# Kernel tuning notes

Hardware: AMD Instinct MI355X
Metric: run time of the kernel (lower is better)

## Reference

```python
import jax, jax.numpy as jnp
import numpy as np

N = 50000      # nodes
E = 300000     # edges
B = 256        # graphs
F = 128        # feat_dim
F2 = 256       # gnn width = 2*feat_dim
Q = 64         # qubit_num
A = 2016       # action_num
L = 10         # SAGEConv layers
NEG = 0.01     # leaky_relu slope
EPS = 1e-5


def _leaky(v):
    return jnp.where(v > 0, v, NEG * v)


def setup_inputs() -> dict:
    key = jax.random.key(0)
    ks = jax.random.split(key, 16)
    s = 0.05
    x = jax.random.randint(ks[0], (N, 2), 0, Q + 1)
    edge_index = jax.random.randint(ks[1], (2, E), 0, N)
    batch = jnp.sort(jax.random.randint(ks[2], (N,), 0, B))
    emb = (jax.random.normal(ks[3], (Q + 1, F)) * s).at[0].set(0.0)  # padding_idx=0
    Wl = jax.random.normal(ks[4], (L, F2, F2)) * s   # SAGEConv lin_l (neighbor)
    bl = jnp.zeros((L, F2))
    Wr = jax.random.normal(ks[5], (L, F2, F2)) * s   # SAGEConv lin_r (root), no bias
    gn_weight = jnp.ones((F2,))
    gn_bias = jnp.zeros((F2,))
    gn_scale = jnp.ones((F2,))                        # GraphNorm mean_scale
    t = jnp.array(1.0, dtype=jnp.float32)             # SoftmaxAggregation temperature
    W1 = jax.random.normal(ks[6], (F2, F2)) * s
    b1 = jnp.zeros((F2,))
    W2 = jax.random.normal(ks[7], (F2, F)) * s
    b2 = jnp.zeros((F,))
    W3 = jax.random.normal(ks[8], (F, A)) * s
    b3 = jnp.zeros((A,))
    return dict(x=x, edge_index=edge_index, batch=batch, emb=emb, Wl=Wl, bl=bl,
                Wr=Wr, gn_weight=gn_weight, gn_bias=gn_bias, gn_scale=gn_scale,
                t=t, W1=W1, b1=b1, W2=W2, b2=b2, W3=W3, b3=b3)


def reference(x, edge_index, batch, emb, Wl, bl, Wr, gn_weight, gn_bias,
              gn_scale, t, W1, b1, W2, b2, W3, b3):
    # node embedding: two qubit tokens per node -> [N, 2F] = [N, F2]
    h = emb.at[0].set(0.0)[x].reshape(-1, F2)
    src, dst = edge_index[0], edge_index[1]
    deg = jax.ops.segment_sum(jnp.ones((E,), h.dtype), dst, num_segments=N)
    deg = jnp.maximum(deg, 1.0)[:, None]
    for i in range(L):
        agg = jax.ops.segment_sum(h[src], dst, num_segments=N) / deg  # [N, F2]
        h2 = agg @ Wl[i] + bl[i] + h @ Wr[i]
        h = _leaky(h2) + h2
    # GraphNorm (per-graph mean/var with learnable mean_scale)
    cnt = jnp.maximum(jax.ops.segment_sum(jnp.ones((N,), h.dtype), batch,
                                          num_segments=B), 1.0)[:, None]
    mean = jax.ops.segment_sum(h, batch, num_segments=B) / cnt
    o = h - mean[batch] * gn_scale
    var = jax.ops.segment_sum(o * o, batch, num_segments=B) / cnt
    h = gn_weight * o / jnp.sqrt(var + EPS)[batch] + gn_bias
    # SoftmaxAggregation (per-graph, per-channel segment softmax weights)
    logits = h * t
    m = jax.ops.segment_max(logits, batch, num_segments=B)
    ex = jnp.exp(logits - m[batch])
    den = jax.ops.segment_sum(ex, batch, num_segments=B)
    alpha = ex / den[batch]
    g = jax.ops.segment_sum(alpha * h, batch, num_segments=B)  # [B, F2]
    # MLP head
    y = _leaky(g @ W1 + b1)
    y = _leaky(y @ W2 + b2)
    return y @ W3 + b3  # [B, A]
```

## Files before the change

kernel.cpp:

```cpp
#include <hip/hip_runtime.h>

typedef unsigned short u16;
typedef __bf16 bf16x8 __attribute__((ext_vector_type(8)));
typedef float floatx4 __attribute__((ext_vector_type(4)));

#define NN 50000
#define EE 300000
#define BB 256
#define MPAD 50048
#define CAP 32
#define AA 2016
#define EB ((EE + 255) / 256)

__device__ __forceinline__ float b2f(u16 u) {
    union { float f; unsigned int i; } x; x.i = ((unsigned int)u) << 16; return x.f;
}
__device__ __forceinline__ float lo16(unsigned int w) {
    union { float f; unsigned int i; } x; x.i = w << 16; return x.f;
}
__device__ __forceinline__ float hi16(unsigned int w) {
    union { float f; unsigned int i; } x; x.i = w & 0xffff0000u; return x.f;
}
__device__ __forceinline__ u16 f2b(float f) {
    union { float f; unsigned int i; } x; x.f = f;
    unsigned int r = (x.i + 0x7fffu + ((x.i >> 16) & 1u)) >> 16;
    return (u16)r;
}
__device__ __forceinline__ int sniff(const u16* tp) {
    return (tp[0] == 0x3F80u) ? 0 : 1;
}
__device__ __forceinline__ float loadf(const void* p, size_t i, int md) {
    return md ? ((const float*)p)[i] : b2f(((const u16*)p)[i]);
}

typedef const void __attribute__((address_space(1)))* gas_ptr;
typedef void __attribute__((address_space(3)))* las_ptr;
#define ASYNC_COPY16(gp, lp) \
    __builtin_amdgcn_global_load_lds((gas_ptr)(const void*)(gp), (las_ptr)(void*)(lp), 16, 0, 0)

__global__ __launch_bounds__(256) void embed_kernel(const int* __restrict__ x,
                                                    const void* __restrict__ emb,
                                                    const u16* __restrict__ tp,
                                                    u16* __restrict__ h,
                                                    int* __restrict__ cur) {
    int md = sniff(tp);
    int idx = blockIdx.x * 256 + threadIdx.x;
    if (idx < NN) cur[idx] = 0;
    int n = idx >> 6, lane = idx & 63;
    int c4 = lane * 4;
    int which = (c4 >> 7) & 1;
    int tok = x[n * 2 + which];
    int ec = c4 & 127;
    size_t ei = (size_t)tok * 128 + ec;
    float e0, e1, e2, e3;
    if (md) {
        float4 v = *(const float4*)((const float*)emb + ei);
        e0 = v.x; e1 = v.y; e2 = v.z; e3 = v.w;
    } else {
        ushort4 v = *(const ushort4*)((const u16*)emb + ei);
        e0 = b2f(v.x); e1 = b2f(v.y); e2 = b2f(v.z); e3 = b2f(v.w);
    }
    ushort4 o;
    o.x = f2b(e0); o.y = f2b(e1); o.z = f2b(e2); o.w = f2b(e3);
    *(ushort4*)&h[(size_t)n * 256 + c4] = o;
}

__global__ __launch_bounds__(256) void scatter_kernel(const int* __restrict__ src,
                                                      const int* __restrict__ dst,
                                                      const int* __restrict__ batch,
                                                      int* __restrict__ cur,
                                                      int* __restrict__ csrc,
                                                      int* __restrict__ goff) {
    int i = blockIdx.x * 256 + threadIdx.x;
    if (i < EE) {
        int d = dst[i];
        int slot = atomicAdd(&cur[d], 1);
        if (slot < CAP) csrc[(size_t)d * CAP + slot] = src[i];
    }
    if (blockIdx.x == EB) {
        for (int t = threadIdx.x; t <= BB; t += 256) {
            int lo = 0, hi = NN;
            while (lo < hi) {
                int mid = (lo + hi) >> 1;
                if (batch[mid] < t) lo = mid + 1; else hi = mid;
            }
            goff[t] = lo;
        }
    }
}

__global__ __launch_bounds__(256) void transpose_kernel(const void* __restrict__ Wl,
                                                        const void* __restrict__ Wr,
                                                        const u16* __restrict__ tp,
                                                        u16* __restrict__ Wt) {
    __shared__ float tile[32][33];
    int md = sniff(tp);
    int w2 = blockIdx.z;
    const void* Ws = (w2 & 1) ? Wr : Wl;
    size_t base = (size_t)(w2 >> 1) * 65536;
    u16* Wo = Wt + (size_t)w2 * 65536;
    int kt = blockIdx.y * 32, nt = blockIdx.x * 32;
    int tx = threadIdx.x, ty = threadIdx.y;
#pragma unroll
    for (int q = 0; q < 4; ++q)
        tile[ty + q * 8][tx] = loadf(Ws, base + (size_t)(kt + ty + q * 8) * 256 + nt + tx, md);
    __syncthreads();
#pragma unroll
    for (int q = 0; q < 4; ++q)
        Wo[(size_t)(nt + ty + q * 8) * 256 + kt + tx] = f2b(tile[tx][ty + q * 8]);
}

__global__ __launch_bounds__(256) void agg_kernel(const u16* __restrict__ h,
                                                  const int* __restrict__ cur,
                                                  const int* __restrict__ csrc,
                                                  u16* __restrict__ agg) {
    int node = blockIdx.x * 4 + (threadIdx.x >> 6);
    int lane = threadIdx.x & 63;
    int half = lane >> 5, l32 = lane & 31;
    int cd = cur[node];
    float id = 1.0f / (float)(cd > 1 ? cd : 1);
    int cnt = cd > CAP ? CAP : cd;
    const int s = node * CAP;
    const int e = s + cnt;
    float a[8] = {};
    int p = s + half;
    for (; p + 2 < e; p += 4) {
        int sn0 = csrc[p];
        int sn1 = csrc[p + 2];
        uint4 h0 = *(const uint4*)&h[(size_t)sn0 * 256 + l32 * 8];
        uint4 h1 = *(const uint4*)&h[(size_t)sn1 * 256 + l32 * 8];
        a[0] += lo16(h0.x) + lo16(h1.x); a[1] += hi16(h0.x) + hi16(h1.x);
        a[2] += lo16(h0.y) + lo16(h1.y); a[3] += hi16(h0.y) + hi16(h1.y);
        a[4] += lo16(h0.z) + lo16(h1.z); a[5] += hi16(h0.z) + hi16(h1.z);
        a[6] += lo16(h0.w) + lo16(h1.w); a[7] += hi16(h0.w) + hi16(h1.w);
    }
    if (p < e) {
        int sn = csrc[p];
        uint4 hv = *(const uint4*)&h[(size_t)sn * 256 + l32 * 8];
        a[0] += lo16(hv.x); a[1] += hi16(hv.x);
        a[2] += lo16(hv.y); a[3] += hi16(hv.y);
        a[4] += lo16(hv.z); a[5] += hi16(hv.z);
        a[6] += lo16(hv.w); a[7] += hi16(hv.w);
    }
#pragma unroll
    for (int j = 0; j < 8; ++j) a[j] += __shfl_xor(a[j], 32, 64);
    if (half == 0) {
        u16 o[8];
#pragma unroll
        for (int j = 0; j < 8; ++j) o[j] = f2b(a[j] * id);
        *(uint4*)&agg[(size_t)node * 256 + l32 * 8] = *(uint4*)o;
    }
}

__global__ __launch_bounds__(512, 4) void gemm_kernel(const u16* __restrict__ A0,
                                                      const u16* __restrict__ A1,
                                                      const u16* __restrict__ B0,
                                                      const u16* __restrict__ B1,
                                                      const void* __restrict__ blv,
                                                      int layer,
                                                      const u16* __restrict__ tp,
                                                      u16* __restrict__ Hout) {
    __shared__ __align__(16) u16 As[2][128 * 32];
    __shared__ __align__(16) u16 Bs[2][256 * 32];
    int md = sniff(tp);
    const int tid = threadIdx.x;
    const int lane = tid & 63;
    const int wv = tid >> 6;
    const int wm = wv >> 2, wn = wv & 3;
    const int m0 = blockIdx.x * 128;
    const int r16 = lane & 15, q = lane >> 4;
    const int rg = lane >> 2;
    const int slot = lane & 3;

    floatx4 acc[4][4] = {};

    auto issue = [&](int kt, int p) {
        const u16* __restrict__ Asrc = (kt < 8) ? A0 : A1;
        const u16* __restrict__ Bsrc = (kt < 8) ? B0 : B1;
        const int koff = (kt & 7) * 32;
        {
            int row = wv * 16 + rg;
            int g = slot ^ ((row >> 1) & 3);
            int ga = m0 + row; if (ga > NN - 1) ga = NN - 1;
            ASYNC_COPY16(Asrc + (size_t)ga * 256 + koff + g * 8,
                         &As[p][(wv * 16) * 32]);
        }
#pragma unroll
        for (int i = 0; i < 2; ++i) {
            int row = wv * 32 + i * 16 + rg;
            int g = slot ^ ((row >> 1) & 3);
            ASYNC_COPY16(Bsrc + (size_t)row * 256 + koff + g * 8,
                         &Bs[p][(wv * 32 + i * 16) * 32]);
        }
    };

    issue(0, 0);
    for (int kt = 0; kt < 16; ++kt) {
        __syncthreads();
        if (kt < 15) issue(kt + 1, (kt + 1) & 1);
        const int p = kt & 1;
        bf16x8 av[4], bv[4];
#pragma unroll
        for (int mt = 0; mt < 4; ++mt) {
            int row = wm * 64 + mt * 16 + r16;
            int pc = q ^ ((row >> 1) & 3);
            av[mt] = *(const bf16x8*)&As[p][row * 32 + pc * 8];
        }
#pragma unroll
        for (int nt = 0; nt < 4; ++nt) {
            int row = wn * 64 + nt * 16 + r16;
            int pc = q ^ ((row >> 1) & 3);
            bv[nt] = *(const bf16x8*)&Bs[p][row * 32 + pc * 8];
        }
#pragma unroll
        for (int mt = 0; mt < 4; ++mt)
#pragma unroll
            for (int nt = 0; nt < 4; ++nt)
                acc[mt][nt] = __builtin_amdgcn_mfma_f32_16x16x32_bf16(
                    bv[nt], av[mt], acc[mt][nt], 0, 0, 0);
    }
#pragma unroll
    for (int nt = 0; nt < 4; ++nt) {
        int gn = wn * 64 + nt * 16 + q * 4;
        float b0 = loadf(blv, (size_t)layer * 256 + gn + 0, md);
        float b1 = loadf(blv, (size_t)layer * 256 + gn + 1, md);
        float b2 = loadf(blv, (size_t)layer * 256 + gn + 2, md);
        float b3 = loadf(blv, (size_t)layer * 256 + gn + 3, md);
#pragma unroll
        for (int mt = 0; mt < 4; ++mt) {
            int gm = m0 + wm * 64 + mt * 16 + r16;
            if (gm < NN) {
                float v0 = acc[mt][nt][0] + b0;
                float v1 = acc[mt][nt][1] + b1;
                float v2 = acc[mt][nt][2] + b2;
                float v3 = acc[mt][nt][3] + b3;
                v0 = (v0 > 0.f) ? 2.f * v0 : 1.01f * v0;
                v1 = (v1 > 0.f) ? 2.f * v1 : 1.01f * v1;
                v2 = (v2 > 0.f) ? 2.f * v2 : 1.01f * v2;
                v3 = (v3 > 0.f) ? 2.f * v3 : 1.01f * v3;
                ushort4 o;
                o.x = f2b(v0); o.y = f2b(v1); o.z = f2b(v2); o.w = f2b(v3);
                *(ushort4*)&Hout[(size_t)gm * 256 + gn] = o;
            }
        }
    }
}

__global__ __launch_bounds__(1024) void gn_softmax_kernel(const u16* __restrict__ h,
                                                          const int* __restrict__ goff,
                                                          const void* __restrict__ gnw,
                                                          const void* __restrict__ gnb,
                                                          const void* __restrict__ gns,
                                                          const u16* __restrict__ tp,
                                                          float* __restrict__ g) {
    __shared__ float red[1024];
    __shared__ float red2[1024];
    int md = sniff(tp);
    const int sub = threadIdx.x >> 8;
    const int c = threadIdx.x & 255;
    const int b = blockIdx.x;
    const int s = goff[b], e = goff[b + 1];
    const int cn = e - s;
    const float icnt = 1.0f / (float)(cn > 1 ? cn : 1);

    float sum = 0.f, sq = 0.f;
#pragma unroll 4
    for (int n = s + sub; n < e; n += 4) {
        float hv = b2f(h[(size_t)n * 256 + c]);
        sum += hv; sq += hv * hv;
    }
    red[threadIdx.x] = sum; red2[threadIdx.x] = sq; __syncthreads();
    float mean = (red[c] + red[256 + c] + red[512 + c] + red[768 + c]) * icnt;
    float e2 = (red2[c] + red2[256 + c] + red2[512 + c] + red2[768 + c]) * icnt;
    float msc = mean * loadf(gns, c, md);
    float var = e2 - 2.f * msc * mean + msc * msc;
    if (var < 0.f) var = 0.f;
    float w = loadf(gnw, c, md) * rsqrtf(var + 1e-5f);
    float bb = loadf(gnb, c, md);
    float tv = md ? ((const float*)tp)[0] : b2f(tp[0]);
    __syncthreads();

    float den = 0.f, num = 0.f;
#pragma unroll 4
    for (int n = s + sub; n < e; n += 4) {
        float hn = w * (b2f(h[(size_t)n * 256 + c]) - msc) + bb;
        float elv = __expf(fminf(hn * tv, 60.f));
        den += elv; num += elv * hn;
    }
    red[threadIdx.x] = den; red2[threadIdx.x] = num; __syncthreads();
    if (sub == 0) {
        float D = red[c] + red[256 + c] + red[512 + c] + red[768 + c];
        float Nu = red2[c] + red2[256 + c] + red2[512 + c] + red2[768 + c];
        g[b * 256 + c] = (D > 1e-30f) ? (Nu / D) : 0.f;
    }
}

__global__ __launch_bounds__(256) void y1_kernel(const float* __restrict__ g,
                                                 const void* __restrict__ W1,
                                                 const void* __restrict__ b1,
                                                 const u16* __restrict__ tp,
                                                 float* __restrict__ y1) {
    __shared__ float gr[256];
    int md = sniff(tp);
    int row = blockIdx.x, t = threadIdx.x;
    gr[t] = g[row * 256 + t];
    __syncthreads();
    float acc = 0.f;
    if (md) {
        const float* W = (const float*)W1;
#pragma unroll 8
        for (int k = 0; k < 256; ++k) acc += gr[k] * W[(size_t)k * 256 + t];
    } else {
        const u16* W = (const u16*)W1;
#pragma unroll 8
        for (int k = 0; k < 256; ++k) acc += gr[k] * b2f(W[(size_t)k * 256 + t]);
    }
    float v = acc + loadf(b1, t, md);
    y1[row * 256 + t] = (v > 0.f) ? v : 0.01f * v;
}

__global__ __launch_bounds__(128) void y2_kernel(const float* __restrict__ y1,
                                                 const void* __restrict__ W2,
                                                 const void* __restrict__ b2v,
                                                 const u16* __restrict__ tp,
                                                 float* __restrict__ y2) {
    __shared__ float yr[256];
    int md = sniff(tp);
    int row = blockIdx.x, t = threadIdx.x;
    yr[t] = y1[row * 256 + t];
    yr[t + 128] = y1[row * 256 + t + 128];
    __syncthreads();
    float acc = 0.f;
    if (md) {
        const float* W = (const float*)W2;
#pragma unroll 8
        for (int k = 0; k < 256; ++k) acc += yr[k] * W[(size_t)k * 128 + t];
    } else {
        const u16* W = (const u16*)W2;
#pragma unroll 8
        for (int k = 0; k < 256; ++k) acc += yr[k] * b2f(W[(size_t)k * 128 + t]);
    }
    float v = acc + loadf(b2v, t, md);
    y2[row * 128 + t] = (v > 0.f) ? v : 0.01f * v;
}

__global__ __launch_bounds__(256) void out_kernel(const float* __restrict__ y2,
                                                  const void* __restrict__ W3,
                                                  const void* __restrict__ b3,
                                                  const u16* __restrict__ tp,
                                                  void* __restrict__ outp) {
    __shared__ float yr[128];
    int md = sniff(tp);
    int row = blockIdx.y;
    int col = blockIdx.x * 256 + threadIdx.x;
    if (threadIdx.x < 128) yr[threadIdx.x] = y2[row * 128 + threadIdx.x];
    __syncthreads();
    if (col >= AA) return;
    float acc = 0.f;
    if (md) {
        const float* W = (const float*)W3;
#pragma unroll 8
        for (int k = 0; k < 128; ++k) acc += yr[k] * W[(size_t)k * AA + col];
    } else {
        const u16* W = (const u16*)W3;
#pragma unroll 8
        for (int k = 0; k < 128; ++k) acc += yr[k] * b2f(W[(size_t)k * AA + col]);
    }
    float v = acc + loadf(b3, col, md);
    if (md) ((float*)outp)[(size_t)row * AA + col] = v;
    else    ((u16*)outp)[(size_t)row * AA + col] = f2b(v);
}

extern "C" void kernel_launch(void* const* d_in, const int* in_sizes, int n_in,
                              void* d_out, int out_size, void* d_ws, size_t ws_size,
                              hipStream_t stream) {
    const int* xi    = (const int*)d_in[0];
    const int* ei    = (const int*)d_in[1];
    const int* srcp  = ei;
    const int* dstp  = ei + EE;
    const int* batch = (const int*)d_in[2];
    const void* emb = d_in[3];
    const void* Wl  = d_in[4];
    const void* bl  = d_in[5];
    const void* Wr  = d_in[6];
    const void* gnw = d_in[7];
    const void* gnb = d_in[8];
    const void* gns = d_in[9];
    const u16* tp   = (const u16*)d_in[10];
    const void* W1  = d_in[11];
    const void* b1  = d_in[12];
    const void* W2  = d_in[13];
    const void* b2v = d_in[14];
    const void* W3  = d_in[15];
    const void* b3  = d_in[16];

    unsigned char* ws = (unsigned char*)d_ws;
    size_t off = 0;
    auto alloc = [&](size_t b) -> size_t {
        size_t o = off; off = (off + b + 255) & ~(size_t)255; return o;
    };
    size_t hA_o  = alloc((size_t)MPAD * 256 * 2);
    size_t hB_o  = alloc((size_t)MPAD * 256 * 2);
    size_t agg_o = alloc((size_t)MPAD * 256 * 2);
    size_t Wt_o  = alloc((size_t)20 * 65536 * 2);
    size_t cur_o = alloc((size_t)NN * 4);
    size_t csrc_o = alloc((size_t)NN * CAP * 4);
    size_t goff_o = alloc((size_t)(BB + 1) * 4);
    size_t g_o   = alloc((size_t)BB * 256 * 4);
    size_t y1_o  = alloc((size_t)BB * 256 * 4);
    size_t y2_o  = alloc((size_t)BB * 128 * 4);

    u16* hA   = (u16*)(ws + hA_o);
    u16* hB   = (u16*)(ws + hB_o);
    u16* aggb = (u16*)(ws + agg_o);
    u16* Wt   = (u16*)(ws + Wt_o);
    int* cur  = (int*)(ws + cur_o);
    int* csrc = (int*)(ws + csrc_o);
    int* goff = (int*)(ws + goff_o);
    float* gbuf = (float*)(ws + g_o);
    float* y1b  = (float*)(ws + y1_o);
    float* y2b  = (float*)(ws + y2_o);

    embed_kernel<<<12500, 256, 0, stream>>>(xi, emb, tp, hA, cur);
    transpose_kernel<<<dim3(8, 8, 20), dim3(32, 8), 0, stream>>>(Wl, Wr, tp, Wt);
    scatter_kernel<<<EB + 1, 256, 0, stream>>>(srcp, dstp, batch, cur, csrc, goff);

    u16* hcur = hA;
    u16* hnxt = hB;
    for (int l = 0; l < 10; ++l) {
        agg_kernel<<<12500, 256, 0, stream>>>(hcur, cur, csrc, aggb);
        gemm_kernel<<<391, 512, 0, stream>>>(
            aggb, hcur,
            Wt + (size_t)(2 * l) * 65536, Wt + (size_t)(2 * l + 1) * 65536,
            bl, l, tp, hnxt);
        u16* t2 = hcur; hcur = hnxt; hnxt = t2;
    }

    gn_softmax_kernel<<<BB, 1024, 0, stream>>>(hcur, goff, gnw, gnb, gns, tp, gbuf);
    y1_kernel<<<BB, 256, 0, stream>>>(gbuf, W1, b1, tp, y1b);
    y2_kernel<<<BB, 128, 0, stream>>>(y1b, W2, b2v, tp, y2b);
    out_kernel<<<dim3(8, BB), 256, 0, stream>>>(y2b, W3, b3, tp, d_out);
}
```

Before: 707.0 us.

## Fuse neighbor aggregation into the per-layer GEMM kernel

Removes the separate aggregation launch and has each GEMM block first compute the mean-aggregated rows for its own 128 nodes, writing them to the global agg buffer. A block barrier follows before the tiled GEMM reads those rows back through async copies. This saves ten launches and the dependency bubble between aggregation and GEMM. In exchange, the gather runs with only 391 blocks and one half-wave per node serially over 8 nodes, giving much less memory-level parallelism than the 12500-block version.

```diff
diff --git a/kernel.cpp b/kernel.cpp
--- a/kernel.cpp
+++ b/kernel.cpp
@@ -110,56 +110,16 @@
         Wo[(size_t)(nt + ty + q * 8) * 256 + kt + tx] = f2b(tile[tx][ty + q * 8]);
 }
 
-__global__ __launch_bounds__(256) void agg_kernel(const u16* __restrict__ h,
-                                                  const int* __restrict__ cur,
-                                                  const int* __restrict__ csrc,
-                                                  u16* __restrict__ agg) {
-    int node = blockIdx.x * 4 + (threadIdx.x >> 6);
-    int lane = threadIdx.x & 63;
-    int half = lane >> 5, l32 = lane & 31;
-    int cd = cur[node];
-    float id = 1.0f / (float)(cd > 1 ? cd : 1);
-    int cnt = cd > CAP ? CAP : cd;
-    const int s = node * CAP;
-    const int e = s + cnt;
-    float a[8] = {};
-    int p = s + half;
-    for (; p + 2 < e; p += 4) {
-        int sn0 = csrc[p];
-        int sn1 = csrc[p + 2];
-        uint4 h0 = *(const uint4*)&h[(size_t)sn0 * 256 + l32 * 8];
-        uint4 h1 = *(const uint4*)&h[(size_t)sn1 * 256 + l32 * 8];
-        a[0] += lo16(h0.x) + lo16(h1.x); a[1] += hi16(h0.x) + hi16(h1.x);
-        a[2] += lo16(h0.y) + lo16(h1.y); a[3] += hi16(h0.y) + hi16(h1.y);
-        a[4] += lo16(h0.z) + lo16(h1.z); a[5] += hi16(h0.z) + hi16(h1.z);
-        a[6] += lo16(h0.w) + lo16(h1.w); a[7] += hi16(h0.w) + hi16(h1.w);
-    }
-    if (p < e) {
-        int sn = csrc[p];
-        uint4 hv = *(const uint4*)&h[(size_t)sn * 256 + l32 * 8];
-        a[0] += lo16(hv.x); a[1] += hi16(hv.x);
-        a[2] += lo16(hv.y); a[3] += hi16(hv.y);
-        a[4] += lo16(hv.z); a[5] += hi16(hv.z);
-        a[6] += lo16(hv.w); a[7] += hi16(hv.w);
-    }
-#pragma unroll
-    for (int j = 0; j < 8; ++j) a[j] += __shfl_xor(a[j], 32, 64);
-    if (half == 0) {
-        u16 o[8];
-#pragma unroll
-        for (int j = 0; j < 8; ++j) o[j] = f2b(a[j] * id);
-        *(uint4*)&agg[(size_t)node * 256 + l32 * 8] = *(uint4*)o;
-    }
-}
-
-__global__ __launch_bounds__(512, 4) void gemm_kernel(const u16* __restrict__ A0,
-                                                      const u16* __restrict__ A1,
-                                                      const u16* __restrict__ B0,
-                                                      const u16* __restrict__ B1,
-                                                      const void* __restrict__ blv,
-                                                      int layer,
-                                                      const u16* __restrict__ tp,
-                                                      u16* __restrict__ Hout) {
+__global__ __launch_bounds__(512, 4) void layer_kernel(const u16* __restrict__ h,
+                                                       const int* __restrict__ cur,
+                                                       const int* __restrict__ csrc,
+                                                       u16* __restrict__ aggb,
+                                                       const u16* __restrict__ B0,
+                                                       const u16* __restrict__ B1,
+                                                       const void* __restrict__ blv,
+                                                       int layer,
+                                                       const u16* __restrict__ tp,
+                                                       u16* __restrict__ Hout) {
     __shared__ __align__(16) u16 As[2][128 * 32];
     __shared__ __align__(16) u16 Bs[2][256 * 32];
     int md = sniff(tp);
@@ -172,10 +132,50 @@
     const int rg = lane >> 2;
     const int slot = lane & 3;
 
+    {
+        const int hw = tid >> 5;
+        const int l32i = tid & 31;
+        for (int ni = 0; ni < 8; ++ni) {
+            int node = m0 + hw * 8 + ni;
+            if (node >= NN) break;
+            int cd = cur[node];
+            float id = 1.0f / (float)(cd > 1 ? cd : 1);
+            int cnt = cd > CAP ? CAP : cd;
+            const int s = node * CAP;
+            const int e = s + cnt;
+            float a[8] = {};
+            int p = s;
+            for (; p + 1 < e; p += 2) {
+                int sn0 = csrc[p];
+                int sn1 = csrc[p + 1];
+                uint4 h0 = *(const uint4*)&h[(size_t)sn0 * 256 + l32i * 8];
+                uint4 h1 = *(const uint4*)&h[(size_t)sn1 * 256 + l32i * 8];
+                a[0] += lo16(h0.x) + lo16(h1.x); a[1] += hi16(h0.x) + hi16(h1.x);
+                a[2] += lo16(h0.y) + lo16(h1.y); a[3] += hi16(h0.y) + hi16(h1.y);
+                a[4] += lo16(h0.z) + lo16(h1.z); a[5] += hi16(h0.z) + hi16(h1.z);
+                a[6] += lo16(h0.w) + lo16(h1.w); a[7] += hi16(h0.w) + hi16(h1.w);
+            }
+            if (p < e) {
+                int sn = csrc[p];
+                uint4 hv = *(const uint4*)&h[(size_t)sn * 256 + l32i * 8];
+                a[0] += lo16(hv.x); a[1] += hi16(hv.x);
+                a[2] += lo16(hv.y); a[3] += hi16(hv.y);
+                a[4] += lo16(hv.z); a[5] += hi16(hv.z);
+                a[6] += lo16(hv.w); a[7] += hi16(hv.w);
+            }
+            u16 o[8];
+#pragma unroll
+            for (int j = 0; j < 8; ++j) o[j] = f2b(a[j] * id);
+            *(uint4*)&aggb[(size_t)node * 256 + l32i * 8] = *(uint4*)o;
+        }
+    }
+    __threadfence_block();
+    __syncthreads();
+
     floatx4 acc[4][4] = {};
 
     auto issue = [&](int kt, int p) {
-        const u16* __restrict__ Asrc = (kt < 8) ? A0 : A1;
+        const u16* __restrict__ Asrc = (kt < 8) ? aggb : h;
         const u16* __restrict__ Bsrc = (kt < 8) ? B0 : B1;
         const int koff = (kt & 7) * 32;
         {
@@ -428,9 +428,8 @@
     u16* hcur = hA;
     u16* hnxt = hB;
     for (int l = 0; l < 10; ++l) {
-        agg_kernel<<<12500, 256, 0, stream>>>(hcur, cur, csrc, aggb);
-        gemm_kernel<<<391, 512, 0, stream>>>(
-            aggb, hcur,
+        layer_kernel<<<391, 512, 0, stream>>>(
+            hcur, cur, csrc, aggb,
             Wt + (size_t)(2 * l) * 65536, Wt + (size_t)(2 * l + 1) * 65536,
             bl, l, tp, hnxt);
         u16* t2 = hcur; hcur = hnxt; hnxt = t2;
```

After: 769.5 us. +8.8%, slower.
